# Optimization experiments

Measured on AMD Instinct MI355X. Metric: run time of the kernel, lower is better.

Reference implementation:

```python
import jax, jax.numpy as jnp
import numpy as np

# so(3) generators (3x3x3), L[s, r, a]
L = jnp.array([[[0, 0, 0], [0, 0, -1], [0, 1, 0]],
               [[0, 0, 1], [0, 0, 0], [-1, 0, 0]],
               [[0, -1, 0], [1, 0, 0], [0, 0, 0]]], dtype=jnp.float32)


def setup_inputs() -> dict:
    key = jax.random.key(0)
    B, S, X, Y = 32, 3, 512, 512
    s = jax.random.normal(key, (B, S, X, Y), dtype=jnp.float32)
    # normalize to unit O(3) spins (physically realistic; math identical for any s)
    s = s / jnp.linalg.norm(s, axis=1, keepdims=True)
    t = jnp.ones((1,), dtype=jnp.float32)   # flow time
    c0 = jnp.ones((1,), dtype=jnp.float32)  # learnable coefficient C[0]
    return {"s": s, "t": t, "c0": c0}


def reference(s, t, c0):
    # Psi11t.grad(s, t): flow force of the (psi_1^1)^2 action term.
    # Coeff(t) with EvenOdd=False and cc=[c0] is t * c0.
    coeff = t * c0  # shape [1], broadcasts

    def nbr(x, mu):
        # sum of forward and backward periodic neighbors along lattice axis mu
        return jnp.roll(x, -1, axis=mu) + jnp.roll(x, 1, axis=mu)

    # b[b,x,y] = sum_mu s . (s shifted +/- along mu)
    b = (jnp.einsum('bsxy,bsxy->bxy', s, nbr(s, 2))
         + jnp.einsum('bsxy,bsxy->bxy', s, nbr(s, 3)))

    bs = s * b[:, None]  # [B,3,X,Y]

    # Lsig[b,r,a,x,y] = -sum_s s[b,s,x,y] * L[s,r,a]
    Lsig = -jnp.einsum('bsxy,sra->braxy', s, L)

    Fs = nbr(s, 2) + nbr(s, 3)      # [B,3,X,Y]
    Fbs = nbr(bs, 2) + nbr(bs, 3)   # [B,3,X,Y]

    F = Fs * b[:, None] + Fbs
    F = jnp.einsum('bsaxy,bsxy->baxy', Lsig, F)  # so(3) generator contraction
    return 2.0 * coeff * F
```

## Files before the change

kernel.cpp:

```cpp
#include <hip/hip_runtime.h>

#define NX 512
#define NY 512
#define XY (NX * NY)

typedef float f4 __attribute__((ext_vector_type(4)));

#define GLOBAL_AS __attribute__((address_space(1)))
#define LDS_AS    __attribute__((address_space(3)))

__global__ __launch_bounds__(512, 4) void psi11t_kernel(
    const float* __restrict__ s,
    const float* __restrict__ t,
    const float* __restrict__ c0,
    float* __restrict__ out)
{
    __shared__ __align__(16) float s_lds[3 * 6 * NY];
    __shared__ __align__(16) float b_lds[6 * NY];

    const int D = blockIdx.x;
    const int Lg = (D & 7) * 512 + (D >> 3);
    const int bidx  = Lg >> 7;
    const int strip = Lg & 127;
    const int x0  = strip * 4;
    const int tid = threadIdx.x;
    const int yb  = (tid & 127) * 4;
    const int r   = tid >> 7;
    const int ybm = (yb + NY - 4) & (NY - 1);
    const int ybp = (yb + 4) & (NY - 1);
    const bool lo256 = (tid < 256);

    const float* sb = s + (size_t)bidx * 3 * XY;

    #pragma unroll
    for (int q = 0; q < 4; ++q) {
        const int rl = r + 4 * q;
        const int c  = rl / 6;
        const int rr = rl - 6 * c;
        const int xg = (x0 - 1 + rr) & (NX - 1);
        const float* gp = sb + (size_t)c * XY + (size_t)xg * NY + (((tid + q * 512) & 127) * 4);
        __builtin_amdgcn_global_load_lds(
            (const GLOBAL_AS void*)gp,
            (LDS_AS void*)&s_lds[(size_t)(tid + q * 512) * 4], 16, 0, 0);
    }
    if (lo256) {
        const int rl = (tid >> 7) + 16;
        const int c  = rl / 6;
        const int rr = rl - 6 * c;
        const int xg = (x0 - 1 + rr) & (NX - 1);
        const float* gp = sb + (size_t)c * XY + (size_t)xg * NY + ((tid & 127) * 4);
        __builtin_amdgcn_global_load_lds(
            (const GLOBAL_AS void*)gp,
            (LDS_AS void*)&s_lds[(size_t)(tid + 2048) * 4], 16, 0, 0);
    }

    f4 ge[3];
    if (lo256) {
        const int xe = (tid < 128) ? ((x0 - 2) & (NX - 1)) : ((x0 + 5) & (NX - 1));
        const float* re = sb + (size_t)xe * NY + yb;
        #pragma unroll
        for (int c = 0; c < 3; ++c) ge[c] = *(const f4*)(re + (size_t)c * XY);
    }

    const float coeff = 2.0f * t[0] * c0[0];
    __syncthreads();

    f4 ce[3], up[3], dn[3];
    float pv3[3], nx0[3];
    f4 bc = {0.f, 0.f, 0.f, 0.f};
    #pragma unroll
    for (int c = 0; c < 3; ++c) {
        const float* S1 = &s_lds[(c * 6 + r + 1) * NY];
        up[c] = *(const f4*)&s_lds[(c * 6 + r) * NY + yb];
        ce[c] = *(const f4*)(S1 + yb);
        dn[c] = *(const f4*)&s_lds[(c * 6 + r + 2) * NY + yb];
        const f4 pv = *(const f4*)(S1 + ybm);
        const f4 nx = *(const f4*)(S1 + ybp);
        pv3[c] = pv[3];
        nx0[c] = nx[0];
        const f4 shl = {pv[3], ce[c][0], ce[c][1], ce[c][2]};
        const f4 shr = {ce[c][1], ce[c][2], ce[c][3], nx[0]};
        bc += ce[c] * (up[c] + dn[c] + shl + shr);
    }
    *(f4*)&b_lds[(r + 1) * NY + yb] = bc;

    if (lo256) {
        const int rb = (tid < 128) ? 0 : 5;
        const int ro = (tid < 128) ? 1 : 4;
        f4 acc = {0.f, 0.f, 0.f, 0.f};
        #pragma unroll
        for (int c = 0; c < 3; ++c) {
            const float* S0 = &s_lds[(c * 6 + rb) * NY];
            const f4 c2 = *(const f4*)(S0 + yb);
            const f4 p2 = *(const f4*)(S0 + ybm);
            const f4 n2 = *(const f4*)(S0 + ybp);
            const f4 ot = *(const f4*)&s_lds[(c * 6 + ro) * NY + yb];
            const f4 sl  = {p2[3], c2[0], c2[1], c2[2]};
            const f4 sr2 = {c2[1], c2[2], c2[3], n2[0]};
            acc += c2 * (ge[c] + ot + sl + sr2);
        }
        *(f4*)&b_lds[rb * NY + yb] = acc;
    }
    __syncthreads();

    const float* B1 = &b_lds[(r + 1) * NY];
    const f4 bu = *(const f4*)&b_lds[r * NY + yb];
    const f4 bd = *(const f4*)&b_lds[(r + 2) * NY + yb];
    const f4 bp = *(const f4*)(B1 + ybm);
    const f4 bn = *(const f4*)(B1 + ybp);
    const f4 bshl = {bp[3], bc[0], bc[1], bc[2]};
    const f4 bshr = {bc[1], bc[2], bc[3], bn[0]};

    f4 G[3];
    #pragma unroll
    for (int c = 0; c < 3; ++c) {
        const f4 shl = {pv3[c], ce[c][0], ce[c][1], ce[c][2]};
        const f4 shr = {ce[c][1], ce[c][2], ce[c][3], nx0[c]};
        const f4 Fs = up[c] + dn[c] + shl + shr;
        G[c] = Fs * bc + up[c] * bu + dn[c] * bd + shl * bshl + shr * bshr;
    }

    const f4 o0 = (ce[1] * G[2] - ce[2] * G[1]) * coeff;
    const f4 o1 = (ce[2] * G[0] - ce[0] * G[2]) * coeff;
    const f4 o2 = (ce[0] * G[1] - ce[1] * G[0]) * coeff;

    float* ob = out + (size_t)bidx * 3 * XY + (size_t)(x0 + r) * NY + yb;
    __builtin_nontemporal_store(o0, (f4*)ob);
    __builtin_nontemporal_store(o1, (f4*)(ob + XY));
    __builtin_nontemporal_store(o2, (f4*)(ob + 2 * XY));
}

extern "C" void kernel_launch(void* const* d_in, const int* in_sizes, int n_in,
                              void* d_out, int out_size, void* d_ws, size_t ws_size,
                              hipStream_t stream) {
    const float* s  = (const float*)d_in[0];
    const float* t  = (const float*)d_in[1];
    const float* c0 = (const float*)d_in[2];
    float* out = (float*)d_out;

    psi11t_kernel<<<4096, 512, 0, stream>>>(s, t, c0, out);
}
```

Before: 179.1 us.

## Stream 32-row x-strips per block with rolling 8-row LDS ring buffer

Each block now walks 8 consecutive 4-row x-tiles (32 rows) instead of a single tile, keeping an 8-slot circular LDS buffer of s rows and prefetching the next 4 rows asynchronously while the current tile computes. This removes the redundant halo reads (previously 8 rows loaded per 4 output rows) and overlaps global loads with compute. The grid shrinks to 512 blocks, which lowers parallelism and occupancy slack on a 256-CU device and serializes work within a block behind two barriers per step.

```diff
diff --git a/kernel.cpp b/kernel.cpp
--- a/kernel.cpp
+++ b/kernel.cpp
@@ -15,119 +15,123 @@
     const float* __restrict__ c0,
     float* __restrict__ out)
 {
-    __shared__ __align__(16) float s_lds[3 * 6 * NY];
+    __shared__ __align__(16) float s_lds[3 * 8 * NY];
     __shared__ __align__(16) float b_lds[6 * NY];
 
-    const int D = blockIdx.x;
-    const int Lg = (D & 7) * 512 + (D >> 3);
-    const int bidx  = Lg >> 7;
-    const int strip = Lg & 127;
-    const int x0  = strip * 4;
     const int tid = threadIdx.x;
+    const int r   = tid >> 7;
     const int yb  = (tid & 127) * 4;
-    const int r   = tid >> 7;
     const int ybm = (yb + NY - 4) & (NY - 1);
     const int ybp = (yb + 4) & (NY - 1);
     const bool lo256 = (tid < 256);
 
-    const float* sb = s + (size_t)bidx * 3 * XY;
+    const int xcd = blockIdx.x & 7;
+    const int j   = blockIdx.x >> 3;
+    const int g0  = xcd * 512 + j * 8;
+    const int bidx = g0 >> 7;
+    const int x00  = (g0 & 127) * 4;
+
+    const float* sb  = s   + (size_t)bidx * 3 * XY;
+    float*       ob0 = out + (size_t)bidx * 3 * XY;
 
     #pragma unroll
-    for (int q = 0; q < 4; ++q) {
-        const int rl = r + 4 * q;
-        const int c  = rl / 6;
-        const int rr = rl - 6 * c;
-        const int xg = (x0 - 1 + rr) & (NX - 1);
-        const float* gp = sb + (size_t)c * XY + (size_t)xg * NY + (((tid + q * 512) & 127) * 4);
+    for (int q = 0; q < 6; ++q) {
+        const int c  = q >> 1;
+        const int x  = x00 - 2 + r + 4 * (q & 1) + NX;
+        const int xg = x & (NX - 1);
+        const int sl = x & 7;
         __builtin_amdgcn_global_load_lds(
-            (const GLOBAL_AS void*)gp,
-            (LDS_AS void*)&s_lds[(size_t)(tid + q * 512) * 4], 16, 0, 0);
-    }
-    if (lo256) {
-        const int rl = (tid >> 7) + 16;
-        const int c  = rl / 6;
-        const int rr = rl - 6 * c;
-        const int xg = (x0 - 1 + rr) & (NX - 1);
-        const float* gp = sb + (size_t)c * XY + (size_t)xg * NY + ((tid & 127) * 4);
-        __builtin_amdgcn_global_load_lds(
-            (const GLOBAL_AS void*)gp,
-            (LDS_AS void*)&s_lds[(size_t)(tid + 2048) * 4], 16, 0, 0);
-    }
-
-    f4 ge[3];
-    if (lo256) {
-        const int xe = (tid < 128) ? ((x0 - 2) & (NX - 1)) : ((x0 + 5) & (NX - 1));
-        const float* re = sb + (size_t)xe * NY + yb;
-        #pragma unroll
-        for (int c = 0; c < 3; ++c) ge[c] = *(const f4*)(re + (size_t)c * XY);
+            (const GLOBAL_AS void*)(sb + (size_t)c * XY + (size_t)xg * NY + yb),
+            (LDS_AS void*)&s_lds[(c * 8 + sl) * NY + yb], 16, 0, 0);
     }
 
     const float coeff = 2.0f * t[0] * c0[0];
-    __syncthreads();
 
-    f4 ce[3], up[3], dn[3];
-    float pv3[3], nx0[3];
-    f4 bc = {0.f, 0.f, 0.f, 0.f};
-    #pragma unroll
-    for (int c = 0; c < 3; ++c) {
-        const float* S1 = &s_lds[(c * 6 + r + 1) * NY];
-        up[c] = *(const f4*)&s_lds[(c * 6 + r) * NY + yb];
-        ce[c] = *(const f4*)(S1 + yb);
-        dn[c] = *(const f4*)&s_lds[(c * 6 + r + 2) * NY + yb];
-        const f4 pv = *(const f4*)(S1 + ybm);
-        const f4 nx = *(const f4*)(S1 + ybp);
-        pv3[c] = pv[3];
-        nx0[c] = nx[0];
-        const f4 shl = {pv[3], ce[c][0], ce[c][1], ce[c][2]};
-        const f4 shr = {ce[c][1], ce[c][2], ce[c][3], nx[0]};
-        bc += ce[c] * (up[c] + dn[c] + shl + shr);
-    }
-    *(f4*)&b_lds[(r + 1) * NY + yb] = bc;
+    for (int i = 0; i < 8; ++i) {
+        const int x0 = x00 + 4 * i;
+        __syncthreads();
 
-    if (lo256) {
-        const int rb = (tid < 128) ? 0 : 5;
-        const int ro = (tid < 128) ? 1 : 4;
-        f4 acc = {0.f, 0.f, 0.f, 0.f};
+        const int sU = (x0 + r - 1 + NX) & 7;
+        const int sC = (x0 + r) & 7;
+        const int sD = (x0 + r + 1) & 7;
+        f4 ce[3], up[3], dn[3];
+        float pv3[3], nx0[3];
+        f4 bc = {0.f, 0.f, 0.f, 0.f};
         #pragma unroll
         for (int c = 0; c < 3; ++c) {
-            const float* S0 = &s_lds[(c * 6 + rb) * NY];
-            const f4 c2 = *(const f4*)(S0 + yb);
-            const f4 p2 = *(const f4*)(S0 + ybm);
-            const f4 n2 = *(const f4*)(S0 + ybp);
-            const f4 ot = *(const f4*)&s_lds[(c * 6 + ro) * NY + yb];
-            const f4 sl  = {p2[3], c2[0], c2[1], c2[2]};
-            const f4 sr2 = {c2[1], c2[2], c2[3], n2[0]};
-            acc += c2 * (ge[c] + ot + sl + sr2);
+            const float* SC = &s_lds[(c * 8 + sC) * NY];
+            up[c] = *(const f4*)&s_lds[(c * 8 + sU) * NY + yb];
+            ce[c] = *(const f4*)(SC + yb);
+            dn[c] = *(const f4*)&s_lds[(c * 8 + sD) * NY + yb];
+            const f4 pv = *(const f4*)(SC + ybm);
+            const f4 nx = *(const f4*)(SC + ybp);
+            pv3[c] = pv[3];
+            nx0[c] = nx[0];
+            const f4 shl = {pv[3], ce[c][0], ce[c][1], ce[c][2]};
+            const f4 shr = {ce[c][1], ce[c][2], ce[c][3], nx[0]};
+            bc += ce[c] * (up[c] + dn[c] + shl + shr);
         }
-        *(f4*)&b_lds[rb * NY + yb] = acc;
+        *(f4*)&b_lds[(r + 1) * NY + yb] = bc;
+
+        if (lo256) {
+            const int xh = (tid < 128) ? (x0 - 1 + NX) : (x0 + 4 + NX);
+            const int hC = xh & 7, hU = (xh - 1) & 7, hD = (xh + 1) & 7;
+            const int rb = (tid < 128) ? 0 : 5;
+            f4 acc = {0.f, 0.f, 0.f, 0.f};
+            #pragma unroll
+            for (int c = 0; c < 3; ++c) {
+                const float* SC = &s_lds[(c * 8 + hC) * NY];
+                const f4 c2 = *(const f4*)(SC + yb);
+                const f4 p2 = *(const f4*)(SC + ybm);
+                const f4 n2 = *(const f4*)(SC + ybp);
+                const f4 u2 = *(const f4*)&s_lds[(c * 8 + hU) * NY + yb];
+                const f4 d2 = *(const f4*)&s_lds[(c * 8 + hD) * NY + yb];
+                const f4 sl2 = {p2[3], c2[0], c2[1], c2[2]};
+                const f4 sr2 = {c2[1], c2[2], c2[3], n2[0]};
+                acc += c2 * (u2 + d2 + sl2 + sr2);
+            }
+            *(f4*)&b_lds[rb * NY + yb] = acc;
+        }
+        __syncthreads();
+
+        if (i < 7) {
+            const int x  = x0 + 6 + r;
+            const int xg = x & (NX - 1);
+            const int sl = x & 7;
+            #pragma unroll
+            for (int q = 0; q < 3; ++q) {
+                __builtin_amdgcn_global_load_lds(
+                    (const GLOBAL_AS void*)(sb + (size_t)q * XY + (size_t)xg * NY + yb),
+                    (LDS_AS void*)&s_lds[(q * 8 + sl) * NY + yb], 16, 0, 0);
+            }
+        }
+
+        const float* B1 = &b_lds[(r + 1) * NY];
+        const f4 bu = *(const f4*)&b_lds[r * NY + yb];
+        const f4 bd = *(const f4*)&b_lds[(r + 2) * NY + yb];
+        const f4 bp = *(const f4*)(B1 + ybm);
+        const f4 bn = *(const f4*)(B1 + ybp);
+        const f4 bshl = {bp[3], bc[0], bc[1], bc[2]};
+        const f4 bshr = {bc[1], bc[2], bc[3], bn[0]};
+
+        f4 G[3];
+        #pragma unroll
+        for (int c = 0; c < 3; ++c) {
+            const f4 shl = {pv3[c], ce[c][0], ce[c][1], ce[c][2]};
+            const f4 shr = {ce[c][1], ce[c][2], ce[c][3], nx0[c]};
+            const f4 Fs = up[c] + dn[c] + shl + shr;
+            G[c] = Fs * bc + up[c] * bu + dn[c] * bd + shl * bshl + shr * bshr;
+        }
+
+        const f4 o0 = (ce[1] * G[2] - ce[2] * G[1]) * coeff;
+        const f4 o1 = (ce[2] * G[0] - ce[0] * G[2]) * coeff;
+        const f4 o2 = (ce[0] * G[1] - ce[1] * G[0]) * coeff;
+
+        float* ob = ob0 + (size_t)(x0 + r) * NY + yb;
+        __builtin_nontemporal_store(o0, (f4*)ob);
+        __builtin_nontemporal_store(o1, (f4*)(ob + XY));
+        __builtin_nontemporal_store(o2, (f4*)(ob + 2 * XY));
     }
-    __syncthreads();
-
-    const float* B1 = &b_lds[(r + 1) * NY];
-    const f4 bu = *(const f4*)&b_lds[r * NY + yb];
-    const f4 bd = *(const f4*)&b_lds[(r + 2) * NY + yb];
-    const f4 bp = *(const f4*)(B1 + ybm);
-    const f4 bn = *(const f4*)(B1 + ybp);
-    const f4 bshl = {bp[3], bc[0], bc[1], bc[2]};
-    const f4 bshr = {bc[1], bc[2], bc[3], bn[0]};
-
-    f4 G[3];
-    #pragma unroll
-    for (int c = 0; c < 3; ++c) {
-        const f4 shl = {pv3[c], ce[c][0], ce[c][1], ce[c][2]};
-        const f4 shr = {ce[c][1], ce[c][2], ce[c][3], nx0[c]};
-        const f4 Fs = up[c] + dn[c] + shl + shr;
-        G[c] = Fs * bc + up[c] * bu + dn[c] * bd + shl * bshl + shr * bshr;
-    }
-
-    const f4 o0 = (ce[1] * G[2] - ce[2] * G[1]) * coeff;
-    const f4 o1 = (ce[2] * G[0] - ce[0] * G[2]) * coeff;
-    const f4 o2 = (ce[0] * G[1] - ce[1] * G[0]) * coeff;
-
-    float* ob = out + (size_t)bidx * 3 * XY + (size_t)(x0 + r) * NY + yb;
-    __builtin_nontemporal_store(o0, (f4*)ob);
-    __builtin_nontemporal_store(o1, (f4*)(ob + XY));
-    __builtin_nontemporal_store(o2, (f4*)(ob + 2 * XY));
 }
 
 extern "C" void kernel_launch(void* const* d_in, const int* in_sizes, int n_in,
@@ -138,5 +142,5 @@
     const float* c0 = (const float*)d_in[2];
     float* out = (float*)d_out;
 
-    psi11t_kernel<<<4096, 512, 0, stream>>>(s, t, c0, out);
+    psi11t_kernel<<<512, 512, 0, stream>>>(s, t, c0, out);
 }
```

Result: slower. 184.3 us (+2.9%).

## Process eight rows per block with two rows per thread to cut halo overhead

Applied to the files above, without the earlier changes.

Each block now covers 8 x-rows instead of 4, and each thread computes two adjacent rows. The grid shrinks to 2048 blocks and the LDS tile grows to 10 rows of s plus 10 rows of b. This lowers the halo re-read ratio from 8 loaded rows per 4 output rows to 12 per 8, which cuts redundant global traffic and the cost of the b halo recompute. In exchange it uses more LDS and registers per block, which may reduce occupancy, and it leaves fewer blocks to spread across the CUs.

```diff
diff --git a/kernel.cpp b/kernel.cpp
--- a/kernel.cpp
+++ b/kernel.cpp
@@ -15,17 +15,17 @@
     const float* __restrict__ c0,
     float* __restrict__ out)
 {
-    __shared__ __align__(16) float s_lds[3 * 6 * NY];
-    __shared__ __align__(16) float b_lds[6 * NY];
+    __shared__ __align__(16) float s_lds[3 * 10 * NY];
+    __shared__ __align__(16) float b_lds[10 * NY];
 
-    const int D = blockIdx.x;
-    const int Lg = (D & 7) * 512 + (D >> 3);
-    const int bidx  = Lg >> 7;
-    const int strip = Lg & 127;
-    const int x0  = strip * 4;
+    const int D   = blockIdx.x;
+    const int gid = (D & 7) * 256 + (D >> 3);
+    const int bidx  = gid >> 6;
+    const int strip = gid & 63;
+    const int x0  = strip * 8;
     const int tid = threadIdx.x;
+    const int r   = tid >> 7;
     const int yb  = (tid & 127) * 4;
-    const int r   = tid >> 7;
     const int ybm = (yb + NY - 4) & (NY - 1);
     const int ybp = (yb + 4) & (NY - 1);
     const bool lo256 = (tid < 256);
@@ -33,30 +33,28 @@
     const float* sb = s + (size_t)bidx * 3 * XY;
 
     #pragma unroll
-    for (int q = 0; q < 4; ++q) {
-        const int rl = r + 4 * q;
-        const int c  = rl / 6;
-        const int rr = rl - 6 * c;
-        const int xg = (x0 - 1 + rr) & (NX - 1);
-        const float* gp = sb + (size_t)c * XY + (size_t)xg * NY + (((tid + q * 512) & 127) * 4);
+    for (int q = 0; q < 7; ++q) {
+        const int k  = tid + q * 512;
+        const int ru = k >> 7;
+        const int c  = (ru >= 20) ? 2 : ((ru >= 10) ? 1 : 0);
+        const int sr = ru - 10 * c;
+        const int xg = (x0 - 1 + sr + NX) & (NX - 1);
         __builtin_amdgcn_global_load_lds(
-            (const GLOBAL_AS void*)gp,
-            (LDS_AS void*)&s_lds[(size_t)(tid + q * 512) * 4], 16, 0, 0);
+            (const GLOBAL_AS void*)(sb + (size_t)c * XY + (size_t)xg * NY + (k & 127) * 4),
+            (LDS_AS void*)&s_lds[(size_t)k * 4], 16, 0, 0);
     }
     if (lo256) {
-        const int rl = (tid >> 7) + 16;
-        const int c  = rl / 6;
-        const int rr = rl - 6 * c;
-        const int xg = (x0 - 1 + rr) & (NX - 1);
-        const float* gp = sb + (size_t)c * XY + (size_t)xg * NY + ((tid & 127) * 4);
+        const int k  = tid + 7 * 512;
+        const int sr = (k >> 7) - 20;
+        const int xg = (x0 - 1 + sr) & (NX - 1);
         __builtin_amdgcn_global_load_lds(
-            (const GLOBAL_AS void*)gp,
-            (LDS_AS void*)&s_lds[(size_t)(tid + 2048) * 4], 16, 0, 0);
+            (const GLOBAL_AS void*)(sb + (size_t)2 * XY + (size_t)xg * NY + (k & 127) * 4),
+            (LDS_AS void*)&s_lds[(size_t)k * 4], 16, 0, 0);
     }
 
     f4 ge[3];
     if (lo256) {
-        const int xe = (tid < 128) ? ((x0 - 2) & (NX - 1)) : ((x0 + 5) & (NX - 1));
+        const int xe = (tid < 128) ? ((x0 - 2 + NX) & (NX - 1)) : ((x0 + 9) & (NX - 1));
         const float* re = sb + (size_t)xe * NY + yb;
         #pragma unroll
         for (int c = 0; c < 3; ++c) ge[c] = *(const f4*)(re + (size_t)c * XY);
@@ -65,69 +63,93 @@
     const float coeff = 2.0f * t[0] * c0[0];
     __syncthreads();
 
-    f4 ce[3], up[3], dn[3];
-    float pv3[3], nx0[3];
-    f4 bc = {0.f, 0.f, 0.f, 0.f};
+    f4 up[3], ce0[3], ce1[3], dn[3];
+    float pv30[3], nx00[3], pv31[3], nx01[3];
+    f4 bc0 = {0.f, 0.f, 0.f, 0.f};
+    f4 bc1 = {0.f, 0.f, 0.f, 0.f};
     #pragma unroll
     for (int c = 0; c < 3; ++c) {
-        const float* S1 = &s_lds[(c * 6 + r + 1) * NY];
-        up[c] = *(const f4*)&s_lds[(c * 6 + r) * NY + yb];
-        ce[c] = *(const f4*)(S1 + yb);
-        dn[c] = *(const f4*)&s_lds[(c * 6 + r + 2) * NY + yb];
-        const f4 pv = *(const f4*)(S1 + ybm);
-        const f4 nx = *(const f4*)(S1 + ybp);
-        pv3[c] = pv[3];
-        nx0[c] = nx[0];
-        const f4 shl = {pv[3], ce[c][0], ce[c][1], ce[c][2]};
-        const f4 shr = {ce[c][1], ce[c][2], ce[c][3], nx[0]};
-        bc += ce[c] * (up[c] + dn[c] + shl + shr);
+        const float* S0 = &s_lds[(c * 10 + 2 * r + 1) * NY];
+        const float* S1 = &s_lds[(c * 10 + 2 * r + 2) * NY];
+        up[c]  = *(const f4*)&s_lds[(c * 10 + 2 * r) * NY + yb];
+        ce0[c] = *(const f4*)(S0 + yb);
+        ce1[c] = *(const f4*)(S1 + yb);
+        dn[c]  = *(const f4*)&s_lds[(c * 10 + 2 * r + 3) * NY + yb];
+        const f4 pv0 = *(const f4*)(S0 + ybm);
+        const f4 nx0 = *(const f4*)(S0 + ybp);
+        const f4 pv1 = *(const f4*)(S1 + ybm);
+        const f4 nx1 = *(const f4*)(S1 + ybp);
+        pv30[c] = pv0[3]; nx00[c] = nx0[0];
+        pv31[c] = pv1[3]; nx01[c] = nx1[0];
+        const f4 shl0 = {pv0[3], ce0[c][0], ce0[c][1], ce0[c][2]};
+        const f4 shr0 = {ce0[c][1], ce0[c][2], ce0[c][3], nx0[0]};
+        const f4 shl1 = {pv1[3], ce1[c][0], ce1[c][1], ce1[c][2]};
+        const f4 shr1 = {ce1[c][1], ce1[c][2], ce1[c][3], nx1[0]};
+        bc0 += ce0[c] * (up[c] + ce1[c] + shl0 + shr0);
+        bc1 += ce1[c] * (ce0[c] + dn[c] + shl1 + shr1);
     }
-    *(f4*)&b_lds[(r + 1) * NY + yb] = bc;
+    *(f4*)&b_lds[(2 * r + 1) * NY + yb] = bc0;
+    *(f4*)&b_lds[(2 * r + 2) * NY + yb] = bc1;
 
     if (lo256) {
-        const int rb = (tid < 128) ? 0 : 5;
-        const int ro = (tid < 128) ? 1 : 4;
+        const int br = (tid < 128) ? 0 : 9;
+        const int ro = (tid < 128) ? 1 : 8;
         f4 acc = {0.f, 0.f, 0.f, 0.f};
         #pragma unroll
         for (int c = 0; c < 3; ++c) {
-            const float* S0 = &s_lds[(c * 6 + rb) * NY];
-            const f4 c2 = *(const f4*)(S0 + yb);
-            const f4 p2 = *(const f4*)(S0 + ybm);
-            const f4 n2 = *(const f4*)(S0 + ybp);
-            const f4 ot = *(const f4*)&s_lds[(c * 6 + ro) * NY + yb];
+            const float* SC = &s_lds[(c * 10 + br) * NY];
+            const f4 c2 = *(const f4*)(SC + yb);
+            const f4 p2 = *(const f4*)(SC + ybm);
+            const f4 n2 = *(const f4*)(SC + ybp);
+            const f4 ot = *(const f4*)&s_lds[(c * 10 + ro) * NY + yb];
             const f4 sl  = {p2[3], c2[0], c2[1], c2[2]};
             const f4 sr2 = {c2[1], c2[2], c2[3], n2[0]};
             acc += c2 * (ge[c] + ot + sl + sr2);
         }
-        *(f4*)&b_lds[rb * NY + yb] = acc;
+        *(f4*)&b_lds[br * NY + yb] = acc;
     }
     __syncthreads();
 
-    const float* B1 = &b_lds[(r + 1) * NY];
-    const f4 bu = *(const f4*)&b_lds[r * NY + yb];
-    const f4 bd = *(const f4*)&b_lds[(r + 2) * NY + yb];
-    const f4 bp = *(const f4*)(B1 + ybm);
-    const f4 bn = *(const f4*)(B1 + ybp);
-    const f4 bshl = {bp[3], bc[0], bc[1], bc[2]};
-    const f4 bshr = {bc[1], bc[2], bc[3], bn[0]};
+    const f4 bu0 = *(const f4*)&b_lds[(2 * r) * NY + yb];
+    const f4 bd1 = *(const f4*)&b_lds[(2 * r + 3) * NY + yb];
+    const float* B0 = &b_lds[(2 * r + 1) * NY];
+    const float* B1 = &b_lds[(2 * r + 2) * NY];
+    const f4 bp0 = *(const f4*)(B0 + ybm);
+    const f4 bn0 = *(const f4*)(B0 + ybp);
+    const f4 bp1 = *(const f4*)(B1 + ybm);
+    const f4 bn1 = *(const f4*)(B1 + ybp);
+    const f4 bshl0 = {bp0[3], bc0[0], bc0[1], bc0[2]};
+    const f4 bshr0 = {bc0[1], bc0[2], bc0[3], bn0[0]};
+    const f4 bshl1 = {bp1[3], bc1[0], bc1[1], bc1[2]};
+    const f4 bshr1 = {bc1[1], bc1[2], bc1[3], bn1[0]};
 
-    f4 G[3];
+    f4 G0[3], G1[3];
     #pragma unroll
     for (int c = 0; c < 3; ++c) {
-        const f4 shl = {pv3[c], ce[c][0], ce[c][1], ce[c][2]};
-        const f4 shr = {ce[c][1], ce[c][2], ce[c][3], nx0[c]};
-        const f4 Fs = up[c] + dn[c] + shl + shr;
-        G[c] = Fs * bc + up[c] * bu + dn[c] * bd + shl * bshl + shr * bshr;
+        const f4 shl0 = {pv30[c], ce0[c][0], ce0[c][1], ce0[c][2]};
+        const f4 shr0 = {ce0[c][1], ce0[c][2], ce0[c][3], nx00[c]};
+        const f4 shl1 = {pv31[c], ce1[c][0], ce1[c][1], ce1[c][2]};
+        const f4 shr1 = {ce1[c][1], ce1[c][2], ce1[c][3], nx01[c]};
+        const f4 Fs0 = up[c] + ce1[c] + shl0 + shr0;
+        const f4 Fs1 = ce0[c] + dn[c] + shl1 + shr1;
+        G0[c] = Fs0 * bc0 + up[c]  * bu0 + ce1[c] * bc1 + shl0 * bshl0 + shr0 * bshr0;
+        G1[c] = Fs1 * bc1 + ce0[c] * bc0 + dn[c]  * bd1 + shl1 * bshl1 + shr1 * bshr1;
     }
 
-    const f4 o0 = (ce[1] * G[2] - ce[2] * G[1]) * coeff;
-    const f4 o1 = (ce[2] * G[0] - ce[0] * G[2]) * coeff;
-    const f4 o2 = (ce[0] * G[1] - ce[1] * G[0]) * coeff;
+    const f4 o00 = (ce0[1] * G0[2] - ce0[2] * G0[1]) * coeff;
+    const f4 o01 = (ce0[2] * G0[0] - ce0[0] * G0[2]) * coeff;
+    const f4 o02 = (ce0[0] * G0[1] - ce0[1] * G0[0]) * coeff;
+    const f4 o10 = (ce1[1] * G1[2] - ce1[2] * G1[1]) * coeff;
+    const f4 o11 = (ce1[2] * G1[0] - ce1[0] * G1[2]) * coeff;
+    const f4 o12 = (ce1[0] * G1[1] - ce1[1] * G1[0]) * coeff;
 
-    float* ob = out + (size_t)bidx * 3 * XY + (size_t)(x0 + r) * NY + yb;
-    __builtin_nontemporal_store(o0, (f4*)ob);
-    __builtin_nontemporal_store(o1, (f4*)(ob + XY));
-    __builtin_nontemporal_store(o2, (f4*)(ob + 2 * XY));
+    float* ob = out + (size_t)bidx * 3 * XY + (size_t)(x0 + 2 * r) * NY + yb;
+    __builtin_nontemporal_store(o00, (f4*)ob);
+    __builtin_nontemporal_store(o01, (f4*)(ob + XY));
+    __builtin_nontemporal_store(o02, (f4*)(ob + 2 * XY));
+    __builtin_nontemporal_store(o10, (f4*)(ob + NY));
+    __builtin_nontemporal_store(o11, (f4*)(ob + XY + NY));
+    __builtin_nontemporal_store(o12, (f4*)(ob + 2 * XY + NY));
 }
 
 extern "C" void kernel_launch(void* const* d_in, const int* in_sizes, int n_in,
@@ -138,5 +160,5 @@
     const float* c0 = (const float*)d_in[2];
     float* out = (float*)d_out;
 
-    psi11t_kernel<<<4096, 512, 0, stream>>>(s, t, c0, out);
+    psi11t_kernel<<<2048, 512, 0, stream>>>(s, t, c0, out);
 }
```

After: 201.1 us. 1.12x slower.

## Recompute neighbor b values per thread and split tiles along y with halos

Applied to the files above, without the earlier changes.

Each thread now recomputes the b values of its up, down, left and right neighbors directly from a halo-padded LDS tile, so the b_lds buffer and the second barrier go away. Tiles are split in half along y with 256-thread blocks and 8192 blocks. The LDS footprint is about 25KB, and the separate global edge-row loads are replaced by staging 8 rows per component. In exchange there are more redundant stencil FLOPs and LDS reads per thread, plus halo overhead on y.

```diff
diff --git a/kernel.cpp b/kernel.cpp
--- a/kernel.cpp
+++ b/kernel.cpp
@@ -3,113 +3,104 @@
 #define NX 512
 #define NY 512
 #define XY (NX * NY)
+#define LROW 264
+#define NRC 24
+#define NCHUNK (NRC * 66)
 
 typedef float f4 __attribute__((ext_vector_type(4)));
 
 #define GLOBAL_AS __attribute__((address_space(1)))
 #define LDS_AS    __attribute__((address_space(3)))
 
-__global__ __launch_bounds__(512, 4) void psi11t_kernel(
+__global__ __launch_bounds__(256, 6) void psi11t_kernel(
     const float* __restrict__ s,
     const float* __restrict__ t,
     const float* __restrict__ c0,
     float* __restrict__ out)
 {
-    __shared__ __align__(16) float s_lds[3 * 6 * NY];
-    __shared__ __align__(16) float b_lds[6 * NY];
+    __shared__ __align__(16) float s_lds[NRC * LROW];
 
-    const int D = blockIdx.x;
-    const int Lg = (D & 7) * 512 + (D >> 3);
-    const int bidx  = Lg >> 7;
-    const int strip = Lg & 127;
+    const int D   = blockIdx.x;
+    const int gid = (D & 7) * 1024 + (D >> 3);
+    const int bidx  = gid >> 8;
+    const int half  = (gid >> 7) & 1;
+    const int strip = gid & 127;
     const int x0  = strip * 4;
+    const int yb0 = half * 256;
+
     const int tid = threadIdx.x;
-    const int yb  = (tid & 127) * 4;
-    const int r   = tid >> 7;
-    const int ybm = (yb + NY - 4) & (NY - 1);
-    const int ybp = (yb + 4) & (NY - 1);
-    const bool lo256 = (tid < 256);
+    const int r   = tid >> 6;
+    const int yl  = (tid & 63) * 4;
 
     const float* sb = s + (size_t)bidx * 3 * XY;
 
+    auto stage = [&](int k) {
+        const int rc  = k / 66;
+        const int col = (k - rc * 66) * 4;
+        const int c   = rc >> 3;
+        const int R   = rc & 7;
+        const int xg  = (x0 - 2 + R + NX) & (NX - 1);
+        const int y   = (yb0 - 4 + col + NY) & (NY - 1);
+        __builtin_amdgcn_global_load_lds(
+            (const GLOBAL_AS void*)(sb + (size_t)c * XY + (size_t)xg * NY + y),
+            (LDS_AS void*)&s_lds[rc * LROW + col], 16, 0, 0);
+    };
     #pragma unroll
-    for (int q = 0; q < 4; ++q) {
-        const int rl = r + 4 * q;
-        const int c  = rl / 6;
-        const int rr = rl - 6 * c;
-        const int xg = (x0 - 1 + rr) & (NX - 1);
-        const float* gp = sb + (size_t)c * XY + (size_t)xg * NY + (((tid + q * 512) & 127) * 4);
-        __builtin_amdgcn_global_load_lds(
-            (const GLOBAL_AS void*)gp,
-            (LDS_AS void*)&s_lds[(size_t)(tid + q * 512) * 4], 16, 0, 0);
-    }
-    if (lo256) {
-        const int rl = (tid >> 7) + 16;
-        const int c  = rl / 6;
-        const int rr = rl - 6 * c;
-        const int xg = (x0 - 1 + rr) & (NX - 1);
-        const float* gp = sb + (size_t)c * XY + (size_t)xg * NY + ((tid & 127) * 4);
-        __builtin_amdgcn_global_load_lds(
-            (const GLOBAL_AS void*)gp,
-            (LDS_AS void*)&s_lds[(size_t)(tid + 2048) * 4], 16, 0, 0);
-    }
-
-    f4 ge[3];
-    if (lo256) {
-        const int xe = (tid < 128) ? ((x0 - 2) & (NX - 1)) : ((x0 + 5) & (NX - 1));
-        const float* re = sb + (size_t)xe * NY + yb;
-        #pragma unroll
-        for (int c = 0; c < 3; ++c) ge[c] = *(const f4*)(re + (size_t)c * XY);
-    }
+    for (int q = 0; q < 6; ++q) stage(tid + q * 256);
+    if (tid < 48) stage(tid + 1536);
 
     const float coeff = 2.0f * t[0] * c0[0];
     __syncthreads();
 
-    f4 ce[3], up[3], dn[3];
+    f4 up[3], ce[3], dn[3];
     float pv3[3], nx0[3];
+    f4 bu = {0.f, 0.f, 0.f, 0.f};
     f4 bc = {0.f, 0.f, 0.f, 0.f};
+    f4 bd = {0.f, 0.f, 0.f, 0.f};
+    float bl = 0.f, br = 0.f;
+
     #pragma unroll
     for (int c = 0; c < 3; ++c) {
-        const float* S1 = &s_lds[(c * 6 + r + 1) * NY];
-        up[c] = *(const f4*)&s_lds[(c * 6 + r) * NY + yb];
-        ce[c] = *(const f4*)(S1 + yb);
-        dn[c] = *(const f4*)&s_lds[(c * 6 + r + 2) * NY + yb];
-        const f4 pv = *(const f4*)(S1 + ybm);
-        const f4 nx = *(const f4*)(S1 + ybp);
-        pv3[c] = pv[3];
-        nx0[c] = nx[0];
-        const f4 shl = {pv[3], ce[c][0], ce[c][1], ce[c][2]};
-        const f4 shr = {ce[c][1], ce[c][2], ce[c][3], nx[0]};
-        bc += ce[c] * (up[c] + dn[c] + shl + shr);
+        const float* base = &s_lds[(c * 8) * LROW + 4 + yl];
+        const float* Rm2 = base + (r    ) * LROW;
+        const float* Rm1 = base + (r + 1) * LROW;
+        const float* R0  = base + (r + 2) * LROW;
+        const float* Rp1 = base + (r + 3) * LROW;
+        const float* Rp2 = base + (r + 4) * LROW;
+
+        const f4 ce_m2 = *(const f4*)Rm2;
+        const f4 pv_m1 = *(const f4*)(Rm1 - 4);
+        const f4 ce_m1 = *(const f4*)Rm1;
+        const f4 nx_m1 = *(const f4*)(Rm1 + 4);
+        const f4 pv_0  = *(const f4*)(R0 - 4);
+        const f4 ce_0  = *(const f4*)R0;
+        const f4 nx_0  = *(const f4*)(R0 + 4);
+        const f4 pv_p1 = *(const f4*)(Rp1 - 4);
+        const f4 ce_p1 = *(const f4*)Rp1;
+        const f4 nx_p1 = *(const f4*)(Rp1 + 4);
+        const f4 ce_p2 = *(const f4*)Rp2;
+
+        const f4 shl_m1 = {pv_m1[3], ce_m1[0], ce_m1[1], ce_m1[2]};
+        const f4 shr_m1 = {ce_m1[1], ce_m1[2], ce_m1[3], nx_m1[0]};
+        bu += ce_m1 * (ce_m2 + ce_0 + shl_m1 + shr_m1);
+
+        const f4 shl_0 = {pv_0[3], ce_0[0], ce_0[1], ce_0[2]};
+        const f4 shr_0 = {ce_0[1], ce_0[2], ce_0[3], nx_0[0]};
+        bc += ce_0 * (ce_m1 + ce_p1 + shl_0 + shr_0);
+
+        const f4 shl_p1 = {pv_p1[3], ce_p1[0], ce_p1[1], ce_p1[2]};
+        const f4 shr_p1 = {ce_p1[1], ce_p1[2], ce_p1[3], nx_p1[0]};
+        bd += ce_p1 * (ce_0 + ce_p2 + shl_p1 + shr_p1);
+
+        bl += pv_0[3] * (pv_m1[3] + pv_p1[3] + pv_0[2] + ce_0[0]);
+        br += nx_0[0] * (nx_m1[0] + nx_p1[0] + nx_0[1] + ce_0[3]);
+
+        up[c] = ce_m1; ce[c] = ce_0; dn[c] = ce_p1;
+        pv3[c] = pv_0[3]; nx0[c] = nx_0[0];
     }
-    *(f4*)&b_lds[(r + 1) * NY + yb] = bc;
 
-    if (lo256) {
-        const int rb = (tid < 128) ? 0 : 5;
-        const int ro = (tid < 128) ? 1 : 4;
-        f4 acc = {0.f, 0.f, 0.f, 0.f};
-        #pragma unroll
-        for (int c = 0; c < 3; ++c) {
-            const float* S0 = &s_lds[(c * 6 + rb) * NY];
-            const f4 c2 = *(const f4*)(S0 + yb);
-            const f4 p2 = *(const f4*)(S0 + ybm);
-            const f4 n2 = *(const f4*)(S0 + ybp);
-            const f4 ot = *(const f4*)&s_lds[(c * 6 + ro) * NY + yb];
-            const f4 sl  = {p2[3], c2[0], c2[1], c2[2]};
-            const f4 sr2 = {c2[1], c2[2], c2[3], n2[0]};
-            acc += c2 * (ge[c] + ot + sl + sr2);
-        }
-        *(f4*)&b_lds[rb * NY + yb] = acc;
-    }
-    __syncthreads();
-
-    const float* B1 = &b_lds[(r + 1) * NY];
-    const f4 bu = *(const f4*)&b_lds[r * NY + yb];
-    const f4 bd = *(const f4*)&b_lds[(r + 2) * NY + yb];
-    const f4 bp = *(const f4*)(B1 + ybm);
-    const f4 bn = *(const f4*)(B1 + ybp);
-    const f4 bshl = {bp[3], bc[0], bc[1], bc[2]};
-    const f4 bshr = {bc[1], bc[2], bc[3], bn[0]};
+    const f4 bshl = {bl, bc[0], bc[1], bc[2]};
+    const f4 bshr = {bc[1], bc[2], bc[3], br};
 
     f4 G[3];
     #pragma unroll
@@ -124,7 +115,7 @@
     const f4 o1 = (ce[2] * G[0] - ce[0] * G[2]) * coeff;
     const f4 o2 = (ce[0] * G[1] - ce[1] * G[0]) * coeff;
 
-    float* ob = out + (size_t)bidx * 3 * XY + (size_t)(x0 + r) * NY + yb;
+    float* ob = out + (size_t)bidx * 3 * XY + (size_t)(x0 + r) * NY + yb0 + yl;
     __builtin_nontemporal_store(o0, (f4*)ob);
     __builtin_nontemporal_store(o1, (f4*)(ob + XY));
     __builtin_nontemporal_store(o2, (f4*)(ob + 2 * XY));
@@ -138,5 +129,5 @@
     const float* c0 = (const float*)d_in[2];
     float* out = (float*)d_out;
 
-    psi11t_kernel<<<4096, 512, 0, stream>>>(s, t, c0, out);
+    psi11t_kernel<<<8192, 256, 0, stream>>>(s, t, c0, out);
 }
```

After: 239.1 us. +33.5%, slower.
